# Performance work log

Measured on AMD Instinct MI355X. Metric: run time of the kernel, lower is better.

## Reference

```python
import jax, jax.numpy as jnp
import numpy as np

N, E, D, L, G = 50000, 600000, 128, 4, 128


def setup_inputs() -> dict:
    key = jax.random.key(0)
    ks = jax.random.split(key, 4)
    x = jax.random.normal(ks[0], (N, D), jnp.float32)
    edge_index = jax.random.randint(ks[1], (2, E), 0, N)
    batch = jnp.sort(jax.random.randint(ks[2], (N,), 0, G))
    W = jax.random.normal(ks[3], (L, D, D), jnp.float32) * (1.0 / np.sqrt(D))
    b = jnp.zeros((L, D), jnp.float32)
    gamma = jnp.ones((L, D), jnp.float32)
    beta = jnp.zeros((L, D), jnp.float32)
    return dict(x=x, edge_index=edge_index, batch=batch, W=W, b=b, gamma=gamma, beta=beta)


def _gcn_conv(x, src, dst, W, b):
    """PyG GCNConv: add self-loops, symmetric deg^-1/2 normalization."""
    n = x.shape[0]
    h = x @ W  # [N, D]
    deg = jnp.zeros((n,), x.dtype).at[dst].add(1.0) + 1.0  # +1 for self-loop
    dinv = jax.lax.rsqrt(deg)
    coef = dinv[src] * dinv[dst]  # [E]
    agg = jnp.zeros_like(h).at[dst].add(h[src] * coef[:, None])  # scatter-add messages
    agg = agg + h * (dinv * dinv)[:, None]  # self-loop contribution
    return agg + b


def _layer_norm(x, g, bta, eps=1e-5):
    m = jnp.mean(x, axis=-1, keepdims=True)
    v = jnp.var(x, axis=-1, keepdims=True)
    return (x - m) * jax.lax.rsqrt(v + eps) * g + bta


def reference(x, edge_index, batch, W, b, gamma, beta):
    src, dst = edge_index[0], edge_index[1]
    for l in range(W.shape[0]):  # small fixed layer count
        x = x + _gcn_conv(x, src, dst, W[l], b[l])
        x = _layer_norm(x, gamma[l], beta[l])
        x = jax.nn.relu(x)
    # global mean pool over graphs
    sums = jax.ops.segment_sum(x, batch, num_segments=G)
    cnt = jax.ops.segment_sum(jnp.ones((x.shape[0],), x.dtype), batch, num_segments=G)
    return sums / jnp.clip(cnt, 1.0)[:, None]
```

## Files before the change

### kernel.cpp

```cpp
#include <hip/hip_runtime.h>

#define NN 50000
#define NE 600000
#define DIM 128
#define NLAYER 4
#define NGRAPH 128
#define SCAN_BLOCKS ((NN + 255) / 256)
#define XS_STRIDE 136
#define POOL_SPLIT 4

typedef unsigned int u32;
typedef __attribute__((ext_vector_type(8))) short short8v;
typedef __attribute__((ext_vector_type(4))) float f32x4;

__device__ __forceinline__ u32 bf2(float a, float b) {
    u32 ua = __float_as_uint(a);
    ua = (ua + 0x7fffu + ((ua >> 16) & 1u)) >> 16;
    u32 ub = __float_as_uint(b);
    ub = (ub + 0x7fffu + ((ub >> 16) & 1u)) >> 16;
    return ua | (ub << 16);
}
__device__ __forceinline__ unsigned short bf16r(float a) {
    u32 u = __float_as_uint(a);
    u = (u + 0x7fffu + ((u >> 16) & 1u)) >> 16;
    return (unsigned short)u;
}
__device__ __forceinline__ float bflo(u32 v) { return __uint_as_float(v << 16); }
__device__ __forceinline__ float bfhi(u32 v) { return __uint_as_float(v & 0xffff0000u); }


__global__ void zero2_kernel(int* __restrict__ a, int* __restrict__ b) {
    int i = blockIdx.x * 256 + threadIdx.x;
    if (i < NN) {
        a[i] = 0;
        b[i] = 0;
    }
}

__global__ void deg_kernel(const int* __restrict__ dst, int* __restrict__ deg) {
    int e = blockIdx.x * blockDim.x + threadIdx.x;
    if (e < NE) atomicAdd(&deg[dst[e]], 1);
}

__launch_bounds__(256)
__global__ void blocksum_kernel(const int* __restrict__ deg, int* __restrict__ bsum) {
    int i = blockIdx.x * 256 + threadIdx.x;
    int v = (i < NN) ? deg[i] : 0;
    #pragma unroll
    for (int o = 32; o > 0; o >>= 1) v += __shfl_xor(v, o);
    __shared__ int ws[4];
    int wid = threadIdx.x >> 6;
    if ((threadIdx.x & 63) == 0) ws[wid] = v;
    __syncthreads();
    if (threadIdx.x == 0) bsum[blockIdx.x] = ws[0] + ws[1] + ws[2] + ws[3];
}

__launch_bounds__(256)
__global__ void scanb_kernel(int* __restrict__ bsum) {
    __shared__ int s[256];
    int tid = threadIdx.x;
    int v = (tid < SCAN_BLOCKS) ? bsum[tid] : 0;
    s[tid] = v;
    __syncthreads();
    for (int o = 1; o < 256; o <<= 1) {
        int t = (tid >= o) ? s[tid - o] : 0;
        __syncthreads();
        s[tid] += t;
        __syncthreads();
    }
    if (tid < SCAN_BLOCKS) bsum[tid] = s[tid] - v;
}

__launch_bounds__(256)
__global__ void rowptr_kernel(const int* __restrict__ deg, const int* __restrict__ bsum,
                              int* __restrict__ row_ptr, float* __restrict__ dinv) {
    __shared__ int s[256];
    int tid = threadIdx.x;
    int i = blockIdx.x * 256 + tid;
    int d = (i < NN) ? deg[i] : 0;
    s[tid] = d;
    __syncthreads();
    for (int o = 1; o < 256; o <<= 1) {
        int t = (tid >= o) ? s[tid - o] : 0;
        __syncthreads();
        s[tid] += t;
        __syncthreads();
    }
    if (i < NN) {
        row_ptr[i] = bsum[blockIdx.x] + s[tid] - d;
        dinv[i] = rsqrtf((float)d + 1.0f);
    }
    if (i == 0) row_ptr[NN] = NE;
}

__global__ void fill_kernel(const int* __restrict__ src, const int* __restrict__ dst,
                            const int* __restrict__ row_ptr, int* __restrict__ cnt,
                            int* __restrict__ csr_src) {
    int e = blockIdx.x * blockDim.x + threadIdx.x;
    if (e >= NE) return;
    int d = dst[e];
    int pos = row_ptr[d] + atomicAdd(&cnt[d], 1);
    csr_src[pos] = src[e];
}


__global__ void conv_kernel(const float* __restrict__ x, u32* __restrict__ xb,
                            const float* __restrict__ W, unsigned short* __restrict__ WT) {
    int t = blockIdx.x * 256 + threadIdx.x;
    if (t < NN * 64) {
        float2 v = ((const float2*)x)[t];
        xb[t] = bf2(v.x, v.y);
    } else {
        t -= NN * 64;
        if (t < NLAYER * DIM * DIM) {
            int l = t >> 14;
            int rem = t & 16383;
            int k = rem >> 7, n = rem & 127;
            WT[(size_t)l * 16384 + n * 128 + k] = bf16r(W[(size_t)l * 16384 + k * 128 + n]);
        }
    }
}


__launch_bounds__(256)
__global__ void gemm_mfma_kernel(const u32* __restrict__ Xb, const unsigned short* __restrict__ WTl,
                                 const float* __restrict__ dinv,
                                 unsigned short* __restrict__ H2s, int nrows) {
    __shared__ __align__(16) unsigned short xs[64 * XS_STRIDE];
    __shared__ __align__(16) unsigned short wt[128 * XS_STRIDE];
    const int tid = threadIdx.x;
    const int row0 = blockIdx.x * 64;
    const int nr = min(64, nrows - row0);

    {
        const uint4* xg = (const uint4*)(Xb + (size_t)row0 * 64);
        uint4* xs4 = (uint4*)xs;
        #pragma unroll
        for (int i = 0; i < 4; ++i) {
            int idx = i * 256 + tid;
            int r = idx >> 4, c = idx & 15;
            uint4 v = make_uint4(0u, 0u, 0u, 0u);
            if (r < nr) v = xg[idx];
            xs4[r * 17 + c] = v;
        }
    }
    {
        const uint4* wg = (const uint4*)WTl;
        uint4* wt4 = (uint4*)wt;
        #pragma unroll
        for (int i = 0; i < 8; ++i) {
            int idx = i * 256 + tid;
            int r = idx >> 4, c = idx & 15;
            wt4[r * 17 + c] = wg[idx];
        }
    }
    __syncthreads();

    const int wave = tid >> 6;
    const int lane = tid & 63;
    const int lrow = lane & 15;
    const int kg = lane >> 4;

    short8v a[4];
    #pragma unroll
    for (int kc = 0; kc < 4; ++kc)
        a[kc] = *(const short8v*)&xs[(wave * 16 + lrow) * XS_STRIDE + kc * 32 + kg * 8];

    f32x4 acc[8];
    #pragma unroll
    for (int t = 0; t < 8; ++t) acc[t] = (f32x4){0.f, 0.f, 0.f, 0.f};

    #pragma unroll
    for (int t = 0; t < 8; ++t) {
        #pragma unroll
        for (int kc = 0; kc < 4; ++kc) {
            short8v bfrag = *(const short8v*)&wt[(t * 16 + lrow) * XS_STRIDE + kc * 32 + kg * 8];
            acc[t] = __builtin_amdgcn_mfma_f32_16x16x32_bf16(a[kc], bfrag, acc[t], 0, 0, 0);
        }
    }

    #pragma unroll
    for (int r = 0; r < 4; ++r) {
        int row = row0 + wave * 16 + 4 * kg + r;
        if (row < nrows) {
            float dv = dinv[row];
            #pragma unroll
            for (int t = 0; t < 8; ++t)
                H2s[(size_t)row * DIM + t * 16 + lrow] = bf16r(acc[t][r] * dv);
        }
    }
}


__launch_bounds__(256)
__global__ void gather_ln_kernel(const u32* __restrict__ h2u, const float* __restrict__ dinv,
                                 const int* __restrict__ row_ptr, const int* __restrict__ csr_src,
                                 const float* __restrict__ bl, const float* __restrict__ gamma,
                                 const float* __restrict__ beta, u32* __restrict__ xb) {
    int node = blockIdx.x * 8 + (threadIdx.x >> 5);
    int l = threadIdx.x & 31;
    int beg = row_ptr[node];
    int deg = row_ptr[node + 1] - beg;

    int myidx = (l < deg) ? csr_src[beg + l] : 0;

    uint2 sv = ((const uint2*)(h2u + (size_t)node * 64))[l];
    float a0 = bflo(sv.x), a1 = bfhi(sv.x), a2 = bflo(sv.y), a3 = bfhi(sv.y);
    float c0 = 0.f, c1 = 0.f, c2 = 0.f, c3 = 0.f;

    int e = 0;
    for (; e + 4 <= deg; e += 4) {
        int sn0 = (e     < 32) ? __shfl(myidx, e,     32) : csr_src[beg + e];
        int sn1 = (e + 1 < 32) ? __shfl(myidx, e + 1, 32) : csr_src[beg + e + 1];
        int sn2 = (e + 2 < 32) ? __shfl(myidx, e + 2, 32) : csr_src[beg + e + 2];
        int sn3 = (e + 3 < 32) ? __shfl(myidx, e + 3, 32) : csr_src[beg + e + 3];
        uint2 v0 = ((const uint2*)(h2u + (size_t)sn0 * 64))[l];
        uint2 v1 = ((const uint2*)(h2u + (size_t)sn1 * 64))[l];
        uint2 v2 = ((const uint2*)(h2u + (size_t)sn2 * 64))[l];
        uint2 v3 = ((const uint2*)(h2u + (size_t)sn3 * 64))[l];
        a0 += bflo(v0.x); a1 += bfhi(v0.x); a2 += bflo(v0.y); a3 += bfhi(v0.y);
        c0 += bflo(v1.x); c1 += bfhi(v1.x); c2 += bflo(v1.y); c3 += bfhi(v1.y);
        a0 += bflo(v2.x); a1 += bfhi(v2.x); a2 += bflo(v2.y); a3 += bfhi(v2.y);
        c0 += bflo(v3.x); c1 += bfhi(v3.x); c2 += bflo(v3.y); c3 += bfhi(v3.y);
    }
    for (; e < deg; ++e) {
        int sn = (e < 32) ? __shfl(myidx, e, 32) : csr_src[beg + e];
        uint2 v = ((const uint2*)(h2u + (size_t)sn * 64))[l];
        a0 += bflo(v.x); a1 += bfhi(v.x); a2 += bflo(v.y); a3 += bfhi(v.y);
    }
    a0 += c0; a1 += c1; a2 += c2; a3 += c3;

    float dn = dinv[node];
    uint2 xv = ((const uint2*)(xb + (size_t)node * 64))[l];
    float4 bv = ((const float4*)bl)[l];
    float ax = bflo(xv.x) + a0 * dn + bv.x;
    float ay = bfhi(xv.x) + a1 * dn + bv.y;
    float az = bflo(xv.y) + a2 * dn + bv.z;
    float aw = bfhi(xv.y) + a3 * dn + bv.w;

    float sum = ax + ay + az + aw;
    float sq = ax * ax + ay * ay + az * az + aw * aw;
    #pragma unroll
    for (int o = 16; o > 0; o >>= 1) {
        sum += __shfl_xor(sum, o, 32);
        sq += __shfl_xor(sq, o, 32);
    }
    float mean = sum * (1.0f / DIM);
    float var = sq * (1.0f / DIM) - mean * mean;
    float rstd = rsqrtf(var + 1e-5f);
    float4 g = ((const float4*)gamma)[l];
    float4 bt = ((const float4*)beta)[l];
    float ox = fmaxf((ax - mean) * rstd * g.x + bt.x, 0.f);
    float oy = fmaxf((ay - mean) * rstd * g.y + bt.y, 0.f);
    float oz = fmaxf((az - mean) * rstd * g.z + bt.z, 0.f);
    float ow = fmaxf((aw - mean) * rstd * g.w + bt.w, 0.f);
    uint2 o;
    o.x = bf2(ox, oy);
    o.y = bf2(oz, ow);
    ((uint2*)(xb + (size_t)node * 64))[l] = o;
}


__global__ void bounds_kernel(const int* __restrict__ batch, int* __restrict__ bounds) {
    int g = threadIdx.x;
    if (g > NGRAPH) return;
    int lo = 0, hi = NN;
    while (lo < hi) {
        int mid = (lo + hi) >> 1;
        if (batch[mid] < g) lo = mid + 1; else hi = mid;
    }
    bounds[g] = lo;
}

__launch_bounds__(256)
__global__ void pool1_kernel(const u32* __restrict__ xb, const int* __restrict__ bounds,
                             float* __restrict__ partials) {
    __shared__ float part[3][DIM];
    int g = blockIdx.x >> 2;
    int q = blockIdx.x & 3;
    int beg = bounds[g], end = bounds[g + 1];
    int len = end - beg;
    int qbeg = beg + (int)(((long long)len * q) >> 2);
    int qend = beg + (int)(((long long)len * (q + 1)) >> 2);
    int grp = threadIdx.x >> 6;
    int lane = threadIdx.x & 63;
    float sx = 0.f, sy = 0.f;
    for (int r = qbeg + grp; r < qend; r += 4) {
        u32 v = xb[(size_t)r * 64 + lane];
        sx += bflo(v);
        sy += bfhi(v);
    }
    if (grp > 0) {
        part[grp - 1][lane * 2 + 0] = sx;
        part[grp - 1][lane * 2 + 1] = sy;
    }
    __syncthreads();
    if (grp == 0) {
        sx += part[0][lane * 2] + part[1][lane * 2] + part[2][lane * 2];
        sy += part[0][lane * 2 + 1] + part[1][lane * 2 + 1] + part[2][lane * 2 + 1];
        partials[(size_t)blockIdx.x * DIM + lane * 2 + 0] = sx;
        partials[(size_t)blockIdx.x * DIM + lane * 2 + 1] = sy;
    }
}

__launch_bounds__(256)
__global__ void pool2_kernel(const float* __restrict__ partials, const int* __restrict__ bounds,
                             float* __restrict__ out) {
    int t = blockIdx.x * 256 + threadIdx.x;
    if (t >= NGRAPH * DIM) return;
    int g = t >> 7;
    int d = t & 127;
    float s = partials[(size_t)(4 * g + 0) * DIM + d] + partials[(size_t)(4 * g + 1) * DIM + d] +
              partials[(size_t)(4 * g + 2) * DIM + d] + partials[(size_t)(4 * g + 3) * DIM + d];
    float cntf = (float)(bounds[g + 1] - bounds[g]);
    out[t] = s / fmaxf(cntf, 1.0f);
}


extern "C" void kernel_launch(void* const* d_in, const int* in_sizes, int n_in,
                              void* d_out, int out_size, void* d_ws, size_t ws_size,
                              hipStream_t stream) {
    const float* x     = (const float*)d_in[0];
    const int*   ei    = (const int*)d_in[1];
    const int*   batch = (const int*)d_in[2];
    const float* W     = (const float*)d_in[3];
    const float* b     = (const float*)d_in[4];
    const float* gamma = (const float*)d_in[5];
    const float* beta  = (const float*)d_in[6];
    float* out = (float*)d_out;

    const int* srcE = ei;
    const int* dstE = ei + NE;

    char* p = (char*)d_ws;
    u32*   xb      = (u32*)p;    p += (size_t)NN * (DIM / 2) * sizeof(u32);
    unsigned short* h2s = (unsigned short*)p; p += (size_t)NN * DIM * sizeof(unsigned short);
    unsigned short* WT  = (unsigned short*)p; p += (size_t)NLAYER * DIM * DIM * sizeof(unsigned short);
    float* dinv    = (float*)p;  p += (size_t)NN * sizeof(float);
    int*   deg     = (int*)p;    p += (size_t)NN * sizeof(int);
    int*   ccnt    = (int*)p;    p += (size_t)NN * sizeof(int);
    int*   row_ptr = (int*)p;    p += (size_t)(NN + 1) * sizeof(int);
    int*   csr_src = (int*)p;    p += (size_t)NE * sizeof(int);
    int*   bounds  = (int*)p;    p += (size_t)(NGRAPH + 1) * sizeof(int);
    int*   bsum    = (int*)p;    p += (size_t)SCAN_BLOCKS * sizeof(int);
    float* partials = (float*)p; p += (size_t)NGRAPH * POOL_SPLIT * DIM * sizeof(float);

    zero2_kernel<<<SCAN_BLOCKS, 256, 0, stream>>>(deg, ccnt);
    deg_kernel<<<(NE + 255) / 256, 256, 0, stream>>>(dstE, deg);
    blocksum_kernel<<<SCAN_BLOCKS, 256, 0, stream>>>(deg, bsum);
    scanb_kernel<<<1, 256, 0, stream>>>(bsum);
    rowptr_kernel<<<SCAN_BLOCKS, 256, 0, stream>>>(deg, bsum, row_ptr, dinv);
    fill_kernel<<<(NE + 255) / 256, 256, 0, stream>>>(srcE, dstE, row_ptr, ccnt, csr_src);
    bounds_kernel<<<1, 256, 0, stream>>>(batch, bounds);

    conv_kernel<<<(NN * 64 + NLAYER * DIM * DIM + 255) / 256, 256, 0, stream>>>(x, xb, W, WT);

    for (int l = 0; l < NLAYER; ++l) {
        gemm_mfma_kernel<<<(NN + 63) / 64, 256, 0, stream>>>(
            xb, WT + (size_t)l * DIM * DIM, dinv, h2s, NN);
        gather_ln_kernel<<<NN / 8, 256, 0, stream>>>(
            (const u32*)h2s, dinv, row_ptr, csr_src,
            b + l * DIM, gamma + l * DIM, beta + l * DIM, xb);
    }

    pool1_kernel<<<NGRAPH * POOL_SPLIT, 256, 0, stream>>>(xb, bounds, partials);
    pool2_kernel<<<(NGRAPH * DIM + 255) / 256, 256, 0, stream>>>(partials, bounds, out);
}
```

Baseline: 264.6 us.

## Load GEMM operands directly from global and widen gather to 16-byte loads

The GEMM kernel no longer stages the X tile and W^T in shared memory. Each lane loads its MFMA fragments straight from global memory, which removes the LDS fill, the barrier and the shared-memory footprint, in exchange for repeated global or L2 reads of W per wave. The gather/LayerNorm kernel now uses 16 lanes per node with uint4 (8 bf16) loads instead of 32 lanes with uint2 loads, so each block covers twice as many nodes. This halves the number of memory transactions per gathered row and shortens the shuffle reductions, but increases per-lane register use.

```diff
diff --git a/kernel.cpp b/kernel.cpp
--- a/kernel.cpp
+++ b/kernel.cpp
@@ -6,7 +6,6 @@
 #define NLAYER 4
 #define NGRAPH 128
 #define SCAN_BLOCKS ((NN + 255) / 256)
-#define XS_STRIDE 136
 #define POOL_SPLIT 4
 
 typedef unsigned int u32;
@@ -126,45 +125,19 @@
 __global__ void gemm_mfma_kernel(const u32* __restrict__ Xb, const unsigned short* __restrict__ WTl,
                                  const float* __restrict__ dinv,
                                  unsigned short* __restrict__ H2s, int nrows) {
-    __shared__ __align__(16) unsigned short xs[64 * XS_STRIDE];
-    __shared__ __align__(16) unsigned short wt[128 * XS_STRIDE];
     const int tid = threadIdx.x;
-    const int row0 = blockIdx.x * 64;
-    const int nr = min(64, nrows - row0);
-
-    {
-        const uint4* xg = (const uint4*)(Xb + (size_t)row0 * 64);
-        uint4* xs4 = (uint4*)xs;
-        #pragma unroll
-        for (int i = 0; i < 4; ++i) {
-            int idx = i * 256 + tid;
-            int r = idx >> 4, c = idx & 15;
-            uint4 v = make_uint4(0u, 0u, 0u, 0u);
-            if (r < nr) v = xg[idx];
-            xs4[r * 17 + c] = v;
-        }
-    }
-    {
-        const uint4* wg = (const uint4*)WTl;
-        uint4* wt4 = (uint4*)wt;
-        #pragma unroll
-        for (int i = 0; i < 8; ++i) {
-            int idx = i * 256 + tid;
-            int r = idx >> 4, c = idx & 15;
-            wt4[r * 17 + c] = wg[idx];
-        }
-    }
-    __syncthreads();
-
     const int wave = tid >> 6;
     const int lane = tid & 63;
     const int lrow = lane & 15;
     const int kg = lane >> 4;
 
+    const int row = blockIdx.x * 64 + wave * 16 + lrow;
+    const int arow = min(row, nrows - 1);
+
+    const short8v* xrow = (const short8v*)(Xb + (size_t)arow * 64);
     short8v a[4];
     #pragma unroll
-    for (int kc = 0; kc < 4; ++kc)
-        a[kc] = *(const short8v*)&xs[(wave * 16 + lrow) * XS_STRIDE + kc * 32 + kg * 8];
+    for (int kc = 0; kc < 4; ++kc) a[kc] = xrow[kc * 4 + kg];
 
     f32x4 acc[8];
     #pragma unroll
@@ -172,21 +145,23 @@
 
     #pragma unroll
     for (int t = 0; t < 8; ++t) {
+        const short8v* wrow = (const short8v*)(WTl + (size_t)(t * 16 + lrow) * 128);
         #pragma unroll
         for (int kc = 0; kc < 4; ++kc) {
-            short8v bfrag = *(const short8v*)&wt[(t * 16 + lrow) * XS_STRIDE + kc * 32 + kg * 8];
+            short8v bfrag = wrow[kc * 4 + kg];
             acc[t] = __builtin_amdgcn_mfma_f32_16x16x32_bf16(a[kc], bfrag, acc[t], 0, 0, 0);
         }
     }
 
+    const int rbase = blockIdx.x * 64 + wave * 16 + 4 * kg;
     #pragma unroll
     for (int r = 0; r < 4; ++r) {
-        int row = row0 + wave * 16 + 4 * kg + r;
-        if (row < nrows) {
-            float dv = dinv[row];
+        int orow = rbase + r;
+        if (orow < nrows) {
+            float dv = dinv[orow];
             #pragma unroll
             for (int t = 0; t < 8; ++t)
-                H2s[(size_t)row * DIM + t * 16 + lrow] = bf16r(acc[t][r] * dv);
+                H2s[(size_t)orow * DIM + t * 16 + lrow] = bf16r(acc[t][r] * dv);
         }
     }
 }
@@ -197,67 +172,88 @@
                                  const int* __restrict__ row_ptr, const int* __restrict__ csr_src,
                                  const float* __restrict__ bl, const float* __restrict__ gamma,
                                  const float* __restrict__ beta, u32* __restrict__ xb) {
-    int node = blockIdx.x * 8 + (threadIdx.x >> 5);
-    int l = threadIdx.x & 31;
+    int node = blockIdx.x * 16 + (threadIdx.x >> 4);
+    int l = threadIdx.x & 15;
     int beg = row_ptr[node];
     int deg = row_ptr[node + 1] - beg;
 
     int myidx = (l < deg) ? csr_src[beg + l] : 0;
 
-    uint2 sv = ((const uint2*)(h2u + (size_t)node * 64))[l];
+    const uint4* h4 = (const uint4*)h2u;
+    uint4 sv = h4[(size_t)node * 16 + l];
     float a0 = bflo(sv.x), a1 = bfhi(sv.x), a2 = bflo(sv.y), a3 = bfhi(sv.y);
-    float c0 = 0.f, c1 = 0.f, c2 = 0.f, c3 = 0.f;
+    float a4 = bflo(sv.z), a5 = bfhi(sv.z), a6 = bflo(sv.w), a7 = bfhi(sv.w);
+    float c0 = 0.f, c1 = 0.f, c2 = 0.f, c3 = 0.f, c4 = 0.f, c5 = 0.f, c6 = 0.f, c7 = 0.f;
 
     int e = 0;
     for (; e + 4 <= deg; e += 4) {
-        int sn0 = (e     < 32) ? __shfl(myidx, e,     32) : csr_src[beg + e];
-        int sn1 = (e + 1 < 32) ? __shfl(myidx, e + 1, 32) : csr_src[beg + e + 1];
-        int sn2 = (e + 2 < 32) ? __shfl(myidx, e + 2, 32) : csr_src[beg + e + 2];
-        int sn3 = (e + 3 < 32) ? __shfl(myidx, e + 3, 32) : csr_src[beg + e + 3];
-        uint2 v0 = ((const uint2*)(h2u + (size_t)sn0 * 64))[l];
-        uint2 v1 = ((const uint2*)(h2u + (size_t)sn1 * 64))[l];
-        uint2 v2 = ((const uint2*)(h2u + (size_t)sn2 * 64))[l];
-        uint2 v3 = ((const uint2*)(h2u + (size_t)sn3 * 64))[l];
+        int sn0 = (e     < 16) ? __shfl(myidx, e,     16) : csr_src[beg + e];
+        int sn1 = (e + 1 < 16) ? __shfl(myidx, e + 1, 16) : csr_src[beg + e + 1];
+        int sn2 = (e + 2 < 16) ? __shfl(myidx, e + 2, 16) : csr_src[beg + e + 2];
+        int sn3 = (e + 3 < 16) ? __shfl(myidx, e + 3, 16) : csr_src[beg + e + 3];
+        uint4 v0 = h4[(size_t)sn0 * 16 + l];
+        uint4 v1 = h4[(size_t)sn1 * 16 + l];
+        uint4 v2 = h4[(size_t)sn2 * 16 + l];
+        uint4 v3 = h4[(size_t)sn3 * 16 + l];
         a0 += bflo(v0.x); a1 += bfhi(v0.x); a2 += bflo(v0.y); a3 += bfhi(v0.y);
+        a4 += bflo(v0.z); a5 += bfhi(v0.z); a6 += bflo(v0.w); a7 += bfhi(v0.w);
         c0 += bflo(v1.x); c1 += bfhi(v1.x); c2 += bflo(v1.y); c3 += bfhi(v1.y);
+        c4 += bflo(v1.z); c5 += bfhi(v1.z); c6 += bflo(v1.w); c7 += bfhi(v1.w);
         a0 += bflo(v2.x); a1 += bfhi(v2.x); a2 += bflo(v2.y); a3 += bfhi(v2.y);
+        a4 += bflo(v2.z); a5 += bfhi(v2.z); a6 += bflo(v2.w); a7 += bfhi(v2.w);
         c0 += bflo(v3.x); c1 += bfhi(v3.x); c2 += bflo(v3.y); c3 += bfhi(v3.y);
+        c4 += bflo(v3.z); c5 += bfhi(v3.z); c6 += bflo(v3.w); c7 += bfhi(v3.w);
     }
     for (; e < deg; ++e) {
-        int sn = (e < 32) ? __shfl(myidx, e, 32) : csr_src[beg + e];
-        uint2 v = ((const uint2*)(h2u + (size_t)sn * 64))[l];
+        int sn = (e < 16) ? __shfl(myidx, e, 16) : csr_src[beg + e];
+        uint4 v = h4[(size_t)sn * 16 + l];
         a0 += bflo(v.x); a1 += bfhi(v.x); a2 += bflo(v.y); a3 += bfhi(v.y);
+        a4 += bflo(v.z); a5 += bfhi(v.z); a6 += bflo(v.w); a7 += bfhi(v.w);
     }
     a0 += c0; a1 += c1; a2 += c2; a3 += c3;
+    a4 += c4; a5 += c5; a6 += c6; a7 += c7;
 
     float dn = dinv[node];
-    uint2 xv = ((const uint2*)(xb + (size_t)node * 64))[l];
-    float4 bv = ((const float4*)bl)[l];
-    float ax = bflo(xv.x) + a0 * dn + bv.x;
-    float ay = bfhi(xv.x) + a1 * dn + bv.y;
-    float az = bflo(xv.y) + a2 * dn + bv.z;
-    float aw = bfhi(xv.y) + a3 * dn + bv.w;
-
-    float sum = ax + ay + az + aw;
-    float sq = ax * ax + ay * ay + az * az + aw * aw;
-    #pragma unroll
-    for (int o = 16; o > 0; o >>= 1) {
-        sum += __shfl_xor(sum, o, 32);
-        sq += __shfl_xor(sq, o, 32);
+    uint4 xv = ((const uint4*)xb)[(size_t)node * 16 + l];
+    float4 bv0 = ((const float4*)bl)[2 * l];
+    float4 bv1 = ((const float4*)bl)[2 * l + 1];
+    float e0 = bflo(xv.x) + a0 * dn + bv0.x;
+    float e1 = bfhi(xv.x) + a1 * dn + bv0.y;
+    float e2 = bflo(xv.y) + a2 * dn + bv0.z;
+    float e3 = bfhi(xv.y) + a3 * dn + bv0.w;
+    float e4 = bflo(xv.z) + a4 * dn + bv1.x;
+    float e5 = bfhi(xv.z) + a5 * dn + bv1.y;
+    float e6 = bflo(xv.w) + a6 * dn + bv1.z;
+    float e7 = bfhi(xv.w) + a7 * dn + bv1.w;
+
+    float sum = e0 + e1 + e2 + e3 + e4 + e5 + e6 + e7;
+    float sq = e0 * e0 + e1 * e1 + e2 * e2 + e3 * e3 + e4 * e4 + e5 * e5 + e6 * e6 + e7 * e7;
+    #pragma unroll
+    for (int o = 8; o > 0; o >>= 1) {
+        sum += __shfl_xor(sum, o, 16);
+        sq += __shfl_xor(sq, o, 16);
     }
     float mean = sum * (1.0f / DIM);
     float var = sq * (1.0f / DIM) - mean * mean;
     float rstd = rsqrtf(var + 1e-5f);
-    float4 g = ((const float4*)gamma)[l];
-    float4 bt = ((const float4*)beta)[l];
-    float ox = fmaxf((ax - mean) * rstd * g.x + bt.x, 0.f);
-    float oy = fmaxf((ay - mean) * rstd * g.y + bt.y, 0.f);
-    float oz = fmaxf((az - mean) * rstd * g.z + bt.z, 0.f);
-    float ow = fmaxf((aw - mean) * rstd * g.w + bt.w, 0.f);
-    uint2 o;
-    o.x = bf2(ox, oy);
-    o.y = bf2(oz, ow);
-    ((uint2*)(xb + (size_t)node * 64))[l] = o;
+    float4 g0 = ((const float4*)gamma)[2 * l];
+    float4 g1 = ((const float4*)gamma)[2 * l + 1];
+    float4 t0 = ((const float4*)beta)[2 * l];
+    float4 t1 = ((const float4*)beta)[2 * l + 1];
+    float o0 = fmaxf((e0 - mean) * rstd * g0.x + t0.x, 0.f);
+    float o1 = fmaxf((e1 - mean) * rstd * g0.y + t0.y, 0.f);
+    float o2 = fmaxf((e2 - mean) * rstd * g0.z + t0.z, 0.f);
+    float o3 = fmaxf((e3 - mean) * rstd * g0.w + t0.w, 0.f);
+    float o4 = fmaxf((e4 - mean) * rstd * g1.x + t1.x, 0.f);
+    float o5 = fmaxf((e5 - mean) * rstd * g1.y + t1.y, 0.f);
+    float o6 = fmaxf((e6 - mean) * rstd * g1.z + t1.z, 0.f);
+    float o7 = fmaxf((e7 - mean) * rstd * g1.w + t1.w, 0.f);
+    uint4 ov;
+    ov.x = bf2(o0, o1);
+    ov.y = bf2(o2, o3);
+    ov.z = bf2(o4, o5);
+    ov.w = bf2(o6, o7);
+    ((uint4*)xb)[(size_t)node * 16 + l] = ov;
 }
 
 
@@ -358,7 +354,7 @@
     for (int l = 0; l < NLAYER; ++l) {
         gemm_mfma_kernel<<<(NN + 63) / 64, 256, 0, stream>>>(
             xb, WT + (size_t)l * DIM * DIM, dinv, h2s, NN);
-        gather_ln_kernel<<<NN / 8, 256, 0, stream>>>(
+        gather_ln_kernel<<<NN / 16, 256, 0, stream>>>(
             (const u32*)h2s, dinv, row_ptr, csr_src,
             b + l * DIM, gamma + l * DIM, beta + l * DIM, xb);
     }
```

Result: slower. 293.9 us (+11.1%).
